# Kernel optimization log

Hardware: AMD Instinct MI355X
Metric: run time of the kernel (lower is better)

## Reference

```python
import jax, jax.numpy as jnp
import numpy as np

EPS = 1e-3
MAX_ITER = 100
STAB = 1e-8


def setup_inputs() -> dict:
    key = jax.random.key(0)
    k1, k2 = jax.random.split(key)
    x = jax.random.normal(k1, (4, 4096, 8, 8), dtype=jnp.float32)
    y = jax.random.normal(k2, (4, 4096, 8, 8), dtype=jnp.float32)
    return {"x": x, "y": y}


def _sinkhorn_distance(x, y):
    B, N, H, W = x.shape
    d = H * W
    xf = jax.nn.softmax(x.reshape(B, N, d), axis=-1)  # [B,N,d]
    yf = jax.nn.softmax(y.reshape(B, N, d), axis=-1)  # [B,N,d]

    # squared euclidean distance: ||a-b||^2 = ||a||^2 + ||b||^2 - 2 a.b  (== cdist(p=2)**2)
    x2 = jnp.sum(xf * xf, axis=-1)  # [B,N]
    y2 = jnp.sum(yf * yf, axis=-1)  # [B,N]
    cross = jnp.einsum('bid,bjd->bij', xf, yf)  # [B,N,N]
    cost = jnp.maximum(x2[:, :, None] + y2[:, None, :] - 2.0 * cross, 0.0)

    K = jnp.exp(-cost / EPS)  # [B,N,N]

    u0 = jnp.full((B, N), 1.0 / N, dtype=x.dtype)
    v0 = jnp.full((B, N), 1.0 / N, dtype=x.dtype)

    def step(carry, _):
        u, v = carry
        u = 1.0 / (jnp.einsum('bij,bj->bi', K, v) + STAB)
        v = 1.0 / (jnp.einsum('bij,bi->bj', K, u) + STAB)
        return (u, v), None

    (u, v), _ = jax.lax.scan(step, (u0, v0), None, length=MAX_ITER)

    plan = u[:, :, None] * K * v[:, None, :]  # [B,N,N]
    dist = jnp.sum(plan * cost, axis=(1, 2))  # [B]
    return jnp.sum(dist)  # reduction='sum'


def reference(x, y):
    return _sinkhorn_distance(x, y)
```

## Files before the change

kernel.cpp:

```cpp
#include <hip/hip_runtime.h>
#include <stdint.h>

#define BB 4
#define NN 4096
#define DD 64
#define BN (BB*NN)
#define STABF 1e-8f
#define NITER 100
#define NEG_SCALE (-1442.695040888963f)

__device__ __forceinline__ float bf16lo(uint32_t w){ return __uint_as_float(w << 16); }
__device__ __forceinline__ float bf16hi(uint32_t w){ return __uint_as_float(w & 0xffff0000u); }
__device__ __forceinline__ uint32_t pack2bf(float f0, float f1){
  uint32_t u0 = __float_as_uint(f0); u0 += 0x7fffu + ((u0 >> 16) & 1u);
  uint32_t u1 = __float_as_uint(f1); u1 += 0x7fffu + ((u1 >> 16) & 1u);
  return (u0 >> 16) | (u1 & 0xffff0000u);
}
__device__ __forceinline__ int swz(int c){ return c ^ ((c >> 5) & 7); }

__global__ __launch_bounds__(256) void k_init(float* __restrict__ acc,
                                              float* __restrict__ partial) {
  int idx = blockIdx.x * 256 + threadIdx.x;
  if (idx < BN) {
    acc[idx] = (float)NN;
    acc[BN + idx] = 0.f;
    acc[2 * BN + idx] = 0.f;
  }
  if (idx < 256) partial[idx] = 0.f;
}

__global__ __launch_bounds__(256) void k_softmax(
    const float* __restrict__ x, const float* __restrict__ y,
    float* __restrict__ xf, float* __restrict__ yf,
    float* __restrict__ x2, float* __restrict__ y2) {
  int wave = (blockIdx.x * 256 + threadIdx.x) >> 6;
  int lane = threadIdx.x & 63;
  const float* src; float* dst; float* d2; int row;
  if (wave < BN) { src = x; dst = xf; d2 = x2; row = wave; }
  else           { src = y; dst = yf; d2 = y2; row = wave - BN; }
  float v = src[(size_t)row * DD + lane];
  float m = v;
  #pragma unroll
  for (int off = 32; off; off >>= 1) m = fmaxf(m, __shfl_xor(m, off));
  float e = __expf(v - m);
  float s = e;
  #pragma unroll
  for (int off = 32; off; off >>= 1) s += __shfl_xor(s, off);
  float p = e / s;
  dst[(size_t)row * DD + lane] = p;
  float q = p * p;
  #pragma unroll
  for (int off = 32; off; off >>= 1) q += __shfl_xor(q, off);
  if (lane == 0) d2[row] = q;
}

__device__ __forceinline__ void fma_row(float av0, float av1, const float4 bv,
                                        float cr0[4], float cr1[4]) {
  cr0[0] = fmaf(av0, bv.x, cr0[0]); cr0[1] = fmaf(av0, bv.y, cr0[1]);
  cr0[2] = fmaf(av0, bv.z, cr0[2]); cr0[3] = fmaf(av0, bv.w, cr0[3]);
  cr1[0] = fmaf(av1, bv.x, cr1[0]); cr1[1] = fmaf(av1, bv.y, cr1[1]);
  cr1[2] = fmaf(av1, bv.z, cr1[2]); cr1[3] = fmaf(av1, bv.w, cr1[3]);
}

__global__ __launch_bounds__(256) void k_build(
    const float* __restrict__ xf, const float* __restrict__ yf,
    const float* __restrict__ x2, const float* __restrict__ y2,
    unsigned short* __restrict__ K) {
  __shared__ float sxf[32][68];
  __shared__ float syt[64][68];
  int bid = blockIdx.x, t = threadIdx.x;
  int jt = bid & 63, it = (bid >> 6) & 127, b = bid >> 13;
  int i0 = it * 32, j0 = jt * 64;
  {
    int r = t >> 3, c = (t & 7) * 8;
    const float* s0 = xf + ((size_t)(b*NN + i0 + r)) * DD + c;
    *(float4*)&sxf[r][c]     = *(const float4*)s0;
    *(float4*)&sxf[r][c + 4] = *(const float4*)(s0 + 4);
  }
  {
    int r = t >> 2, c0 = (t & 3) * 16;
    const float* s0 = yf + ((size_t)(b*NN + j0 + r)) * DD + c0;
    #pragma unroll
    for (int q = 0; q < 4; ++q) {
      float4 pv = *(const float4*)(s0 + q*4);
      syt[c0 + q*4 + 0][r] = pv.x;
      syt[c0 + q*4 + 1][r] = pv.y;
      syt[c0 + q*4 + 2][r] = pv.z;
      syt[c0 + q*4 + 3][r] = pv.w;
    }
  }
  __syncthreads();
  int tx = t & 15, ty = t >> 4;
  int ii = ty * 2, jj = tx * 4;
  float cr[2][4] = {{0,0,0,0},{0,0,0,0}};
  #pragma unroll
  for (int d = 0; d < DD; d += 4) {
    float4 a0 = *(const float4*)&sxf[ii][d];
    float4 a1 = *(const float4*)&sxf[ii + 1][d];
    float4 b0 = *(const float4*)&syt[d][jj];
    float4 b1 = *(const float4*)&syt[d + 1][jj];
    float4 b2 = *(const float4*)&syt[d + 2][jj];
    float4 b3 = *(const float4*)&syt[d + 3][jj];
    fma_row(a0.x, a1.x, b0, cr[0], cr[1]);
    fma_row(a0.y, a1.y, b1, cr[0], cr[1]);
    fma_row(a0.z, a1.z, b2, cr[0], cr[1]);
    fma_row(a0.w, a1.w, b3, cr[0], cr[1]);
  }
  float x2v[2], y2v[4];
  x2v[0] = x2[b*NN + i0 + ii]; x2v[1] = x2[b*NN + i0 + ii + 1];
  #pragma unroll
  for (int c = 0; c < 4; ++c) y2v[c] = y2[b*NN + j0 + jj + c];
  #pragma unroll
  for (int i2 = 0; i2 < 2; ++i2) {
    float k4[4];
    #pragma unroll
    for (int c = 0; c < 4; ++c) {
      float cost = fmaxf(x2v[i2] + y2v[c] - 2.f * cr[i2][c], 0.f);
      k4[c] = exp2f(cost * NEG_SCALE);
    }
    uint2 kw;
    kw.x = pack2bf(k4[0], k4[1]);
    kw.y = pack2bf(k4[2], k4[3]);
    *(uint2*)(K + ((size_t)(b*NN + i0 + ii + i2)) * NN + j0 + jj) = kw;
  }
}

__global__ __launch_bounds__(256, 2) void k_iter(
    const unsigned short* __restrict__ K,
    const float* __restrict__ accIn,
    float* __restrict__ accOut,
    float* __restrict__ accZ,
    float* __restrict__ u) {
  __shared__ float sacc[NN];
  int bid = blockIdx.x, t = threadIdx.x;
  int wv = t >> 6, lane = t & 63;
  if (bid < 16) {
    *(float4*)(accZ + (size_t)(bid * 256 + t) * 4) = make_float4(0.f, 0.f, 0.f, 0.f);
  }
  #pragma unroll
  for (int q = 0; q < 16; ++q) sacc[q * 256 + t] = 0.f;

  int b = bid >> 7;
  int row0 = (bid & 127) * 32 + wv * 8;
  const float* ap = accIn + (size_t)b * NN + lane * 8;
  float vv[64];
  #pragma unroll
  for (int itn = 0; itn < 8; ++itn) {
    float4 a0 = *(const float4*)(ap + itn * 512);
    float4 a1 = *(const float4*)(ap + itn * 512 + 4);
    vv[itn*8+0] = __builtin_amdgcn_rcpf(a0.x + STABF);
    vv[itn*8+1] = __builtin_amdgcn_rcpf(a0.y + STABF);
    vv[itn*8+2] = __builtin_amdgcn_rcpf(a0.z + STABF);
    vv[itn*8+3] = __builtin_amdgcn_rcpf(a0.w + STABF);
    vv[itn*8+4] = __builtin_amdgcn_rcpf(a1.x + STABF);
    vv[itn*8+5] = __builtin_amdgcn_rcpf(a1.y + STABF);
    vv[itn*8+6] = __builtin_amdgcn_rcpf(a1.z + STABF);
    vv[itn*8+7] = __builtin_amdgcn_rcpf(a1.w + STABF);
  }
  float ca[64];
  #pragma unroll
  for (int q = 0; q < 64; ++q) ca[q] = 0.f;
  __syncthreads();

  const unsigned short* Kbase = K + (size_t)(b * NN + row0) * NN + lane * 8;
  float* urow = u + b * NN + row0;
  #pragma unroll 1
  for (int r = 0; r < 8; ++r) {
    const unsigned short* Kp = Kbase + (size_t)r * NN;
    uint4 kw[8];
    #pragma unroll
    for (int itn = 0; itn < 8; ++itn) kw[itn] = *(const uint4*)(Kp + itn * 512);
    float sum = 0.f;
    #pragma unroll
    for (int itn = 0; itn < 8; ++itn) {
      sum = fmaf(bf16lo(kw[itn].x), vv[itn*8+0], sum);
      sum = fmaf(bf16hi(kw[itn].x), vv[itn*8+1], sum);
      sum = fmaf(bf16lo(kw[itn].y), vv[itn*8+2], sum);
      sum = fmaf(bf16hi(kw[itn].y), vv[itn*8+3], sum);
      sum = fmaf(bf16lo(kw[itn].z), vv[itn*8+4], sum);
      sum = fmaf(bf16hi(kw[itn].z), vv[itn*8+5], sum);
      sum = fmaf(bf16lo(kw[itn].w), vv[itn*8+6], sum);
      sum = fmaf(bf16hi(kw[itn].w), vv[itn*8+7], sum);
    }
    #pragma unroll
    for (int off = 32; off; off >>= 1) sum += __shfl_xor(sum, off);
    float ur = 1.0f / (sum + STABF);
    if (lane == 0) urow[r] = ur;
    #pragma unroll
    for (int itn = 0; itn < 8; ++itn) {
      ca[itn*8+0] = fmaf(bf16lo(kw[itn].x), ur, ca[itn*8+0]);
      ca[itn*8+1] = fmaf(bf16hi(kw[itn].x), ur, ca[itn*8+1]);
      ca[itn*8+2] = fmaf(bf16lo(kw[itn].y), ur, ca[itn*8+2]);
      ca[itn*8+3] = fmaf(bf16hi(kw[itn].y), ur, ca[itn*8+3]);
      ca[itn*8+4] = fmaf(bf16lo(kw[itn].z), ur, ca[itn*8+4]);
      ca[itn*8+5] = fmaf(bf16hi(kw[itn].z), ur, ca[itn*8+5]);
      ca[itn*8+6] = fmaf(bf16lo(kw[itn].w), ur, ca[itn*8+6]);
      ca[itn*8+7] = fmaf(bf16hi(kw[itn].w), ur, ca[itn*8+7]);
    }
  }
  int cbase = lane * 8;
  #pragma unroll
  for (int itn = 0; itn < 8; ++itn) {
    #pragma unroll
    for (int q = 0; q < 8; ++q)
      atomicAdd(&sacc[swz(itn * 512 + cbase + q)], ca[itn*8+q]);
  }
  __syncthreads();
  float* op = accOut + (size_t)b * NN;
  #pragma unroll
  for (int q = 0; q < 16; ++q) {
    int c = q * 256 + t;
    atomicAdd(op + c, sacc[swz(c)]);
  }
}

__global__ __launch_bounds__(256) void k_final(
    const float* __restrict__ xf, const float* __restrict__ yf,
    const float* __restrict__ x2, const float* __restrict__ y2,
    const unsigned short* __restrict__ K, const float* __restrict__ u,
    const float* __restrict__ accv, float* __restrict__ partial) {
  __shared__ float sxf[32][68];
  __shared__ float syt[64][68];
  __shared__ float red[256];
  int bid = blockIdx.x, t = threadIdx.x;
  int jt = bid & 63, it = (bid >> 6) & 127, b = bid >> 13;
  int i0 = it * 32, j0 = jt * 64;
  {
    int r = t >> 3, c = (t & 7) * 8;
    const float* s0 = xf + ((size_t)(b*NN + i0 + r)) * DD + c;
    *(float4*)&sxf[r][c]     = *(const float4*)s0;
    *(float4*)&sxf[r][c + 4] = *(const float4*)(s0 + 4);
  }
  {
    int r = t >> 2, c0 = (t & 3) * 16;
    const float* s0 = yf + ((size_t)(b*NN + j0 + r)) * DD + c0;
    #pragma unroll
    for (int q = 0; q < 4; ++q) {
      float4 pv = *(const float4*)(s0 + q*4);
      syt[c0 + q*4 + 0][r] = pv.x;
      syt[c0 + q*4 + 1][r] = pv.y;
      syt[c0 + q*4 + 2][r] = pv.z;
      syt[c0 + q*4 + 3][r] = pv.w;
    }
  }
  __syncthreads();
  int tx = t & 15, ty = t >> 4;
  int ii = ty * 2, jj = tx * 4;
  float cr[2][4] = {{0,0,0,0},{0,0,0,0}};
  #pragma unroll
  for (int d = 0; d < DD; d += 4) {
    float4 a0 = *(const float4*)&sxf[ii][d];
    float4 a1 = *(const float4*)&sxf[ii + 1][d];
    float4 b0 = *(const float4*)&syt[d][jj];
    float4 b1 = *(const float4*)&syt[d + 1][jj];
    float4 b2 = *(const float4*)&syt[d + 2][jj];
    float4 b3 = *(const float4*)&syt[d + 3][jj];
    fma_row(a0.x, a1.x, b0, cr[0], cr[1]);
    fma_row(a0.y, a1.y, b1, cr[0], cr[1]);
    fma_row(a0.z, a1.z, b2, cr[0], cr[1]);
    fma_row(a0.w, a1.w, b3, cr[0], cr[1]);
  }
  float x2v[2], y2v[4], uv[2], vv[4];
  x2v[0] = x2[b*NN + i0 + ii]; x2v[1] = x2[b*NN + i0 + ii + 1];
  uv[0]  = u[b*NN + i0 + ii];  uv[1]  = u[b*NN + i0 + ii + 1];
  #pragma unroll
  for (int c = 0; c < 4; ++c) {
    y2v[c] = y2[b*NN + j0 + jj + c];
    vv[c]  = __builtin_amdgcn_rcpf(accv[b*NN + j0 + jj + c] + STABF);
  }
  float s = 0.f;
  #pragma unroll
  for (int i2 = 0; i2 < 2; ++i2) {
    uint2 kw = *(const uint2*)(K + ((size_t)(b*NN + i0 + ii + i2)) * NN + j0 + jj);
    float kk[4] = {bf16lo(kw.x), bf16hi(kw.x), bf16lo(kw.y), bf16hi(kw.y)};
    #pragma unroll
    for (int c = 0; c < 4; ++c) {
      float cost = fmaxf(x2v[i2] + y2v[c] - 2.f * cr[i2][c], 0.f);
      s = fmaf(uv[i2] * kk[c] * vv[c], cost, s);
    }
  }
  red[t] = s;
  __syncthreads();
  #pragma unroll
  for (int off = 128; off; off >>= 1) {
    if (t < off) red[t] += red[t + off];
    __syncthreads();
  }
  if (t == 0) atomicAdd(partial + (bid & 255), red[0]);
}

__global__ __launch_bounds__(256) void k_finalize(const float* __restrict__ partial,
                                                 float* __restrict__ out) {
  __shared__ float red[256];
  int t = threadIdx.x;
  red[t] = partial[t];
  __syncthreads();
  #pragma unroll
  for (int off = 128; off; off >>= 1) {
    if (t < off) red[t] += red[t + off];
    __syncthreads();
  }
  if (t == 0) out[0] = red[0];
}

extern "C" void kernel_launch(void* const* d_in, const int* in_sizes, int n_in,
                              void* d_out, int out_size, void* d_ws, size_t ws_size,
                              hipStream_t stream) {
  const float* x = (const float*)d_in[0];
  const float* y = (const float*)d_in[1];
  float* out = (float*)d_out;

  char* w = (char*)d_ws;
  unsigned short* K = (unsigned short*)w;
  float* xf = (float*)(w + (size_t)BN * NN * 2);
  float* yf = xf + (size_t)BN * DD;
  float* x2 = yf + (size_t)BN * DD;
  float* y2 = x2 + BN;
  float* uu = y2 + BN;
  float* acc = uu + BN;
  float* partial = acc + 3 * BN;
  (void)in_sizes; (void)n_in; (void)out_size; (void)ws_size;

  k_init<<<64, 256, 0, stream>>>(acc, partial);
  k_softmax<<<8192, 256, 0, stream>>>(x, y, xf, yf, x2, y2);
  k_build<<<32768, 256, 0, stream>>>(xf, yf, x2, y2, K);

  for (int itr = 0; itr < NITER; ++itr) {
    int rB = itr % 3, wB = (itr + 1) % 3, zB = (itr + 2) % 3;
    k_iter<<<512, 256, 0, stream>>>(K,
                                    acc + (size_t)rB * BN,
                                    acc + (size_t)wB * BN,
                                    acc + (size_t)zB * BN,
                                    uu);
  }
  k_final<<<32768, 256, 0, stream>>>(xf, yf, x2, y2, K, uu, acc + BN, partial);
  k_finalize<<<1, 256, 0, stream>>>(partial, out);
}
```

Baseline: 6.842 ms.

## Replace global atomics in Sinkhorn iteration with per-block partials plus reduce kernel

Each iteration block now writes its column sums to a private partials slice, and a separate reduce kernel sums the 128 partials per batch and takes the reciprocal to produce v directly. This removes the global float atomics and the triple-buffered zeroing scheme. In exchange there is a second kernel launch per iteration and extra partial-buffer traffic (8 MB written and read per iteration). The old atomic path is kept as a fallback when the workspace is too small.

```diff
diff --git a/kernel.cpp b/kernel.cpp
--- a/kernel.cpp
+++ b/kernel.cpp
@@ -5,6 +5,7 @@
 #define NN 4096
 #define DD 64
 #define BN (BB*NN)
+#define NPB 128
 #define STABF 1e-8f
 #define NITER 100
 #define NEG_SCALE (-1442.695040888963f)
@@ -19,12 +20,14 @@
 __device__ __forceinline__ int swz(int c){ return c ^ ((c >> 5) & 7); }
 
 __global__ __launch_bounds__(256) void k_init(float* __restrict__ acc,
+                                              float* __restrict__ v,
                                               float* __restrict__ partial) {
   int idx = blockIdx.x * 256 + threadIdx.x;
   if (idx < BN) {
     acc[idx] = (float)NN;
     acc[BN + idx] = 0.f;
     acc[2 * BN + idx] = 0.f;
+    v[idx] = 1.0f / (float)NN;
   }
   if (idx < 256) partial[idx] = 0.f;
 }
@@ -127,6 +130,102 @@
 
 __global__ __launch_bounds__(256, 2) void k_iter(
     const unsigned short* __restrict__ K,
+    const float* __restrict__ vIn,
+    float* __restrict__ partials,
+    float* __restrict__ u) {
+  __shared__ float sacc[NN];
+  int bid = blockIdx.x, t = threadIdx.x;
+  int wv = t >> 6, lane = t & 63;
+  #pragma unroll
+  for (int q = 0; q < 16; ++q) sacc[q * 256 + t] = 0.f;
+
+  int b = bid >> 7, pb = bid & 127;
+  int row0 = pb * 32 + wv * 8;
+  const float* vp = vIn + (size_t)b * NN + lane * 8;
+  float vv[64];
+  #pragma unroll
+  for (int itn = 0; itn < 8; ++itn) {
+    float4 a0 = *(const float4*)(vp + itn * 512);
+    float4 a1 = *(const float4*)(vp + itn * 512 + 4);
+    vv[itn*8+0] = a0.x; vv[itn*8+1] = a0.y; vv[itn*8+2] = a0.z; vv[itn*8+3] = a0.w;
+    vv[itn*8+4] = a1.x; vv[itn*8+5] = a1.y; vv[itn*8+6] = a1.z; vv[itn*8+7] = a1.w;
+  }
+  float ca[64];
+  #pragma unroll
+  for (int q = 0; q < 64; ++q) ca[q] = 0.f;
+  __syncthreads();
+
+  const unsigned short* Kbase = K + (size_t)(b * NN + row0) * NN + lane * 8;
+  float* urow = u + b * NN + row0;
+  #pragma unroll 1
+  for (int r = 0; r < 8; ++r) {
+    const unsigned short* Kp = Kbase + (size_t)r * NN;
+    uint4 kw[8];
+    #pragma unroll
+    for (int itn = 0; itn < 8; ++itn) kw[itn] = *(const uint4*)(Kp + itn * 512);
+    float s0 = 0.f, s1 = 0.f, s2 = 0.f, s3 = 0.f;
+    #pragma unroll
+    for (int itn = 0; itn < 8; ++itn) {
+      s0 = fmaf(bf16lo(kw[itn].x), vv[itn*8+0], s0);
+      s1 = fmaf(bf16hi(kw[itn].x), vv[itn*8+1], s1);
+      s2 = fmaf(bf16lo(kw[itn].y), vv[itn*8+2], s2);
+      s3 = fmaf(bf16hi(kw[itn].y), vv[itn*8+3], s3);
+      s0 = fmaf(bf16lo(kw[itn].z), vv[itn*8+4], s0);
+      s1 = fmaf(bf16hi(kw[itn].z), vv[itn*8+5], s1);
+      s2 = fmaf(bf16lo(kw[itn].w), vv[itn*8+6], s2);
+      s3 = fmaf(bf16hi(kw[itn].w), vv[itn*8+7], s3);
+    }
+    float sum = (s0 + s1) + (s2 + s3);
+    #pragma unroll
+    for (int off = 32; off; off >>= 1) sum += __shfl_xor(sum, off);
+    float ur = 1.0f / (sum + STABF);
+    if (lane == 0) urow[r] = ur;
+    #pragma unroll
+    for (int itn = 0; itn < 8; ++itn) {
+      ca[itn*8+0] = fmaf(bf16lo(kw[itn].x), ur, ca[itn*8+0]);
+      ca[itn*8+1] = fmaf(bf16hi(kw[itn].x), ur, ca[itn*8+1]);
+      ca[itn*8+2] = fmaf(bf16lo(kw[itn].y), ur, ca[itn*8+2]);
+      ca[itn*8+3] = fmaf(bf16hi(kw[itn].y), ur, ca[itn*8+3]);
+      ca[itn*8+4] = fmaf(bf16lo(kw[itn].z), ur, ca[itn*8+4]);
+      ca[itn*8+5] = fmaf(bf16hi(kw[itn].z), ur, ca[itn*8+5]);
+      ca[itn*8+6] = fmaf(bf16lo(kw[itn].w), ur, ca[itn*8+6]);
+      ca[itn*8+7] = fmaf(bf16hi(kw[itn].w), ur, ca[itn*8+7]);
+    }
+  }
+  int cbase = lane * 8;
+  #pragma unroll
+  for (int itn = 0; itn < 8; ++itn) {
+    #pragma unroll
+    for (int q = 0; q < 8; ++q)
+      atomicAdd(&sacc[swz(itn * 512 + cbase + q)], ca[itn*8+q]);
+  }
+  __syncthreads();
+  float* op = partials + ((size_t)(b * NPB + pb)) * NN;
+  #pragma unroll
+  for (int q = 0; q < 16; ++q) {
+    int c = q * 256 + t;
+    op[c] = sacc[swz(c)];
+  }
+}
+
+__global__ __launch_bounds__(256) void k_reduce(
+    const float* __restrict__ partials, float* __restrict__ vOut) {
+  int idx = blockIdx.x * 256 + threadIdx.x;
+  int b = idx >> 12, c = idx & (NN - 1);
+  const float* pp = partials + (size_t)b * NPB * NN + c;
+  float s0 = 0.f, s1 = 0.f, s2 = 0.f, s3 = 0.f;
+  #pragma unroll 8
+  for (int p = 0; p < NPB; p += 4) {
+    s0 += pp[(size_t)(p + 0) * NN];
+    s1 += pp[(size_t)(p + 1) * NN];
+    s2 += pp[(size_t)(p + 2) * NN];
+    s3 += pp[(size_t)(p + 3) * NN];
+  }
+  vOut[idx] = 1.0f / (((s0 + s1) + (s2 + s3)) + STABF);
+}
+
+__global__ __launch_bounds__(256, 2) void k_iter_atomic(
+    const unsigned short* __restrict__ K,
     const float* __restrict__ accIn,
     float* __restrict__ accOut,
     float* __restrict__ accZ,
@@ -214,11 +313,17 @@
   }
 }
 
+__global__ __launch_bounds__(256) void k_rcp(const float* __restrict__ acc,
+                                             float* __restrict__ vOut) {
+  int idx = blockIdx.x * 256 + threadIdx.x;
+  vOut[idx] = 1.0f / (acc[idx] + STABF);
+}
+
 __global__ __launch_bounds__(256) void k_final(
     const float* __restrict__ xf, const float* __restrict__ yf,
     const float* __restrict__ x2, const float* __restrict__ y2,
     const unsigned short* __restrict__ K, const float* __restrict__ u,
-    const float* __restrict__ accv, float* __restrict__ partial) {
+    const float* __restrict__ v, float* __restrict__ partial) {
   __shared__ float sxf[32][68];
   __shared__ float syt[64][68];
   __shared__ float red[256];
@@ -266,7 +371,7 @@
   #pragma unroll
   for (int c = 0; c < 4; ++c) {
     y2v[c] = y2[b*NN + j0 + jj + c];
-    vv[c]  = __builtin_amdgcn_rcpf(accv[b*NN + j0 + jj + c] + STABF);
+    vv[c]  = v[b*NN + j0 + jj + c];
   }
   float s = 0.f;
   #pragma unroll
@@ -317,22 +422,34 @@
   float* x2 = yf + (size_t)BN * DD;
   float* y2 = x2 + BN;
   float* uu = y2 + BN;
-  float* acc = uu + BN;
+  float* vb = uu + BN;
+  float* acc = vb + BN;
   float* partial = acc + 3 * BN;
-  (void)in_sizes; (void)n_in; (void)out_size; (void)ws_size;
-
-  k_init<<<64, 256, 0, stream>>>(acc, partial);
+  float* partials = partial + 256;
+  size_t need_fused = (size_t)((char*)(partials + (size_t)BB * NPB * NN) - w);
+  bool fused = (ws_size >= need_fused);
+  (void)in_sizes; (void)n_in; (void)out_size;
+
+  k_init<<<64, 256, 0, stream>>>(acc, vb, partial);
   k_softmax<<<8192, 256, 0, stream>>>(x, y, xf, yf, x2, y2);
   k_build<<<32768, 256, 0, stream>>>(xf, yf, x2, y2, K);
 
-  for (int itr = 0; itr < NITER; ++itr) {
-    int rB = itr % 3, wB = (itr + 1) % 3, zB = (itr + 2) % 3;
-    k_iter<<<512, 256, 0, stream>>>(K,
-                                    acc + (size_t)rB * BN,
-                                    acc + (size_t)wB * BN,
-                                    acc + (size_t)zB * BN,
-                                    uu);
-  }
-  k_final<<<32768, 256, 0, stream>>>(xf, yf, x2, y2, K, uu, acc + BN, partial);
+  if (fused) {
+    for (int itr = 0; itr < NITER; ++itr) {
+      k_iter<<<512, 256, 0, stream>>>(K, vb, partials, uu);
+      k_reduce<<<64, 256, 0, stream>>>(partials, vb);
+    }
+  } else {
+    for (int itr = 0; itr < NITER; ++itr) {
+      int rB = itr % 3, wB = (itr + 1) % 3, zB = (itr + 2) % 3;
+      k_iter_atomic<<<512, 256, 0, stream>>>(K,
+                                             acc + (size_t)rB * BN,
+                                             acc + (size_t)wB * BN,
+                                             acc + (size_t)zB * BN,
+                                             uu);
+    }
+    k_rcp<<<64, 256, 0, stream>>>(acc + BN, vb);
+  }
+  k_final<<<32768, 256, 0, stream>>>(xf, yf, x2, y2, K, uu, vb, partial);
   k_finalize<<<1, 256, 0, stream>>>(partial, out);
 }
```

Result: slower. 7.832 ms (+14.5%).

## Split K_iter columns across waves, double-buffer row batches, drop LDS column reduction

Applied to the files above, without the earlier changes.

Each wave of a block now owns a 1024-column slice instead of 8 whole rows. All four waves work on the same 32 rows, and the per-row partial sums are combined through a tiny LDS buffer with a barrier per 4-row batch. Each thread keeps only 16 column accumulators, so the 4096-float shared column array and its LDS atomics go away, and the thread issues 16 global atomics directly. Row batches are double-buffered in registers so the next loads overlap the current compute. The cost is a block-wide barrier every 4 rows and 16 global atomics per thread that now hit accOut without any block-level pre-reduction.

```diff
diff --git a/kernel.cpp b/kernel.cpp
--- a/kernel.cpp
+++ b/kernel.cpp
@@ -16,7 +16,6 @@
   uint32_t u1 = __float_as_uint(f1); u1 += 0x7fffu + ((u1 >> 16) & 1u);
   return (u0 >> 16) | (u1 & 0xffff0000u);
 }
-__device__ __forceinline__ int swz(int c){ return c ^ ((c >> 5) & 7); }
 
 __global__ __launch_bounds__(256) void k_init(float* __restrict__ acc,
                                               float* __restrict__ partial) {
@@ -125,93 +124,108 @@
   }
 }
 
+__device__ __forceinline__ void loadBatch4(const unsigned short* __restrict__ Kp,
+                                           uint4 kw[8]) {
+  #pragma unroll
+  for (int r = 0; r < 4; ++r) {
+    kw[r*2+0] = *(const uint4*)(Kp + (size_t)r * NN);
+    kw[r*2+1] = *(const uint4*)(Kp + (size_t)r * NN + 8);
+  }
+}
+
+__device__ __forceinline__ void procBatch4(const uint4 kw[8], const float vv[16],
+                                           float ca[16], float* __restrict__ sp,
+                                           float* __restrict__ urow, int bt,
+                                           int wv, int lane) {
+  float d[4];
+  #pragma unroll
+  for (int r = 0; r < 4; ++r) {
+    const uint4 a = kw[r*2], b2 = kw[r*2+1];
+    float s0 = 0.f, s1 = 0.f, s2 = 0.f, s3 = 0.f;
+    s0 = fmaf(bf16lo(a.x),  vv[0],  s0); s1 = fmaf(bf16hi(a.x),  vv[1],  s1);
+    s2 = fmaf(bf16lo(a.y),  vv[2],  s2); s3 = fmaf(bf16hi(a.y),  vv[3],  s3);
+    s0 = fmaf(bf16lo(a.z),  vv[4],  s0); s1 = fmaf(bf16hi(a.z),  vv[5],  s1);
+    s2 = fmaf(bf16lo(a.w),  vv[6],  s2); s3 = fmaf(bf16hi(a.w),  vv[7],  s3);
+    s0 = fmaf(bf16lo(b2.x), vv[8],  s0); s1 = fmaf(bf16hi(b2.x), vv[9],  s1);
+    s2 = fmaf(bf16lo(b2.y), vv[10], s2); s3 = fmaf(bf16hi(b2.y), vv[11], s3);
+    s0 = fmaf(bf16lo(b2.z), vv[12], s0); s1 = fmaf(bf16hi(b2.z), vv[13], s1);
+    s2 = fmaf(bf16lo(b2.w), vv[14], s2); s3 = fmaf(bf16hi(b2.w), vv[15], s3);
+    d[r] = (s0 + s1) + (s2 + s3);
+  }
+  #pragma unroll
+  for (int r = 0; r < 4; ++r) {
+    #pragma unroll
+    for (int off = 32; off; off >>= 1) d[r] += __shfl_xor(d[r], off);
+  }
+  if (lane == 0) {
+    sp[0*4 + wv] = d[0]; sp[1*4 + wv] = d[1];
+    sp[2*4 + wv] = d[2]; sp[3*4 + wv] = d[3];
+  }
+  asm volatile("s_waitcnt lgkmcnt(0)" ::: "memory");
+  __builtin_amdgcn_s_barrier();
+  __builtin_amdgcn_sched_barrier(0);
+  #pragma unroll
+  for (int r = 0; r < 4; ++r) {
+    float4 pr = *(const float4*)&sp[r*4];
+    float ur = 1.0f / (((pr.x + pr.y) + (pr.z + pr.w)) + STABF);
+    if (wv == 0 && lane == 0) urow[bt*4 + r] = ur;
+    const uint4 a = kw[r*2], b2 = kw[r*2+1];
+    ca[0]  = fmaf(bf16lo(a.x),  ur, ca[0]);  ca[1]  = fmaf(bf16hi(a.x),  ur, ca[1]);
+    ca[2]  = fmaf(bf16lo(a.y),  ur, ca[2]);  ca[3]  = fmaf(bf16hi(a.y),  ur, ca[3]);
+    ca[4]  = fmaf(bf16lo(a.z),  ur, ca[4]);  ca[5]  = fmaf(bf16hi(a.z),  ur, ca[5]);
+    ca[6]  = fmaf(bf16lo(a.w),  ur, ca[6]);  ca[7]  = fmaf(bf16hi(a.w),  ur, ca[7]);
+    ca[8]  = fmaf(bf16lo(b2.x), ur, ca[8]);  ca[9]  = fmaf(bf16hi(b2.x), ur, ca[9]);
+    ca[10] = fmaf(bf16lo(b2.y), ur, ca[10]); ca[11] = fmaf(bf16hi(b2.y), ur, ca[11]);
+    ca[12] = fmaf(bf16lo(b2.z), ur, ca[12]); ca[13] = fmaf(bf16hi(b2.z), ur, ca[13]);
+    ca[14] = fmaf(bf16lo(b2.w), ur, ca[14]); ca[15] = fmaf(bf16hi(b2.w), ur, ca[15]);
+  }
+}
+
 __global__ __launch_bounds__(256, 2) void k_iter(
     const unsigned short* __restrict__ K,
     const float* __restrict__ accIn,
     float* __restrict__ accOut,
     float* __restrict__ accZ,
     float* __restrict__ u) {
-  __shared__ float sacc[NN];
+  __shared__ __align__(16) float spart[2][4][4];
   int bid = blockIdx.x, t = threadIdx.x;
   int wv = t >> 6, lane = t & 63;
   if (bid < 16) {
     *(float4*)(accZ + (size_t)(bid * 256 + t) * 4) = make_float4(0.f, 0.f, 0.f, 0.f);
   }
-  #pragma unroll
-  for (int q = 0; q < 16; ++q) sacc[q * 256 + t] = 0.f;
-
   int b = bid >> 7;
-  int row0 = (bid & 127) * 32 + wv * 8;
-  const float* ap = accIn + (size_t)b * NN + lane * 8;
-  float vv[64];
-  #pragma unroll
-  for (int itn = 0; itn < 8; ++itn) {
-    float4 a0 = *(const float4*)(ap + itn * 512);
-    float4 a1 = *(const float4*)(ap + itn * 512 + 4);
-    vv[itn*8+0] = __builtin_amdgcn_rcpf(a0.x + STABF);
-    vv[itn*8+1] = __builtin_amdgcn_rcpf(a0.y + STABF);
-    vv[itn*8+2] = __builtin_amdgcn_rcpf(a0.z + STABF);
-    vv[itn*8+3] = __builtin_amdgcn_rcpf(a0.w + STABF);
-    vv[itn*8+4] = __builtin_amdgcn_rcpf(a1.x + STABF);
-    vv[itn*8+5] = __builtin_amdgcn_rcpf(a1.y + STABF);
-    vv[itn*8+6] = __builtin_amdgcn_rcpf(a1.z + STABF);
-    vv[itn*8+7] = __builtin_amdgcn_rcpf(a1.w + STABF);
-  }
-  float ca[64];
-  #pragma unroll
-  for (int q = 0; q < 64; ++q) ca[q] = 0.f;
-  __syncthreads();
-
-  const unsigned short* Kbase = K + (size_t)(b * NN + row0) * NN + lane * 8;
+  int row0 = (bid & 127) * 32;
+  int colBase = wv * 1024 + lane * 16;
+  const float* ap = accIn + (size_t)b * NN + colBase;
+  float vv[16];
+  #pragma unroll
+  for (int j = 0; j < 4; ++j) {
+    float4 a = *(const float4*)(ap + j * 4);
+    vv[j*4+0] = __builtin_amdgcn_rcpf(a.x + STABF);
+    vv[j*4+1] = __builtin_amdgcn_rcpf(a.y + STABF);
+    vv[j*4+2] = __builtin_amdgcn_rcpf(a.z + STABF);
+    vv[j*4+3] = __builtin_amdgcn_rcpf(a.w + STABF);
+  }
+  float ca[16];
+  #pragma unroll
+  for (int q = 0; q < 16; ++q) ca[q] = 0.f;
+
+  const unsigned short* Kbase = K + (size_t)(b * NN + row0) * NN + colBase;
   float* urow = u + b * NN + row0;
+
+  uint4 kA[8], kB[8];
+  loadBatch4(Kbase, kA);
   #pragma unroll 1
-  for (int r = 0; r < 8; ++r) {
-    const unsigned short* Kp = Kbase + (size_t)r * NN;
-    uint4 kw[8];
-    #pragma unroll
-    for (int itn = 0; itn < 8; ++itn) kw[itn] = *(const uint4*)(Kp + itn * 512);
-    float sum = 0.f;
-    #pragma unroll
-    for (int itn = 0; itn < 8; ++itn) {
-      sum = fmaf(bf16lo(kw[itn].x), vv[itn*8+0], sum);
-      sum = fmaf(bf16hi(kw[itn].x), vv[itn*8+1], sum);
-      sum = fmaf(bf16lo(kw[itn].y), vv[itn*8+2], sum);
-      sum = fmaf(bf16hi(kw[itn].y), vv[itn*8+3], sum);
-      sum = fmaf(bf16lo(kw[itn].z), vv[itn*8+4], sum);
-      sum = fmaf(bf16hi(kw[itn].z), vv[itn*8+5], sum);
-      sum = fmaf(bf16lo(kw[itn].w), vv[itn*8+6], sum);
-      sum = fmaf(bf16hi(kw[itn].w), vv[itn*8+7], sum);
-    }
-    #pragma unroll
-    for (int off = 32; off; off >>= 1) sum += __shfl_xor(sum, off);
-    float ur = 1.0f / (sum + STABF);
-    if (lane == 0) urow[r] = ur;
-    #pragma unroll
-    for (int itn = 0; itn < 8; ++itn) {
-      ca[itn*8+0] = fmaf(bf16lo(kw[itn].x), ur, ca[itn*8+0]);
-      ca[itn*8+1] = fmaf(bf16hi(kw[itn].x), ur, ca[itn*8+1]);
-      ca[itn*8+2] = fmaf(bf16lo(kw[itn].y), ur, ca[itn*8+2]);
-      ca[itn*8+3] = fmaf(bf16hi(kw[itn].y), ur, ca[itn*8+3]);
-      ca[itn*8+4] = fmaf(bf16lo(kw[itn].z), ur, ca[itn*8+4]);
-      ca[itn*8+5] = fmaf(bf16hi(kw[itn].z), ur, ca[itn*8+5]);
-      ca[itn*8+6] = fmaf(bf16lo(kw[itn].w), ur, ca[itn*8+6]);
-      ca[itn*8+7] = fmaf(bf16hi(kw[itn].w), ur, ca[itn*8+7]);
-    }
-  }
-  int cbase = lane * 8;
-  #pragma unroll
-  for (int itn = 0; itn < 8; ++itn) {
-    #pragma unroll
-    for (int q = 0; q < 8; ++q)
-      atomicAdd(&sacc[swz(itn * 512 + cbase + q)], ca[itn*8+q]);
-  }
-  __syncthreads();
-  float* op = accOut + (size_t)b * NN;
-  #pragma unroll
-  for (int q = 0; q < 16; ++q) {
-    int c = q * 256 + t;
-    atomicAdd(op + c, sacc[swz(c)]);
-  }
+  for (int bt = 0; bt < 8; bt += 2) {
+    loadBatch4(Kbase + (size_t)(bt + 1) * 4 * NN, kB);
+    procBatch4(kA, vv, ca, &spart[0][0][0], urow, bt, wv, lane);
+    if (bt < 6) loadBatch4(Kbase + (size_t)(bt + 2) * 4 * NN, kA);
+    procBatch4(kB, vv, ca, &spart[1][0][0], urow, bt + 1, wv, lane);
+  }
+
+  float* op = accOut + (size_t)b * NN + colBase;
+  #pragma unroll
+  for (int c = 0; c < 16; ++c) atomicAdd(op + c, ca[c]);
 }
 
 __global__ __launch_bounds__(256) void k_final(
```

Result: slower. 13.33 ms (+94.8%).
